# Optimization experiments

Hardware: AMD Instinct MI355X
Metric: run time of the kernel (lower is better)

Reference implementation:

```python
import jax, jax.numpy as jnp
import numpy as np

D_MODEL, D_FF, N_EXPERTS, TOP_K = 1024, 4096, 8, 2


def setup_inputs() -> dict:
    key = jax.random.key(0)
    k1, k2, k3, k4 = jax.random.split(key, 4)
    x = jax.random.normal(k1, (2, 2048, D_MODEL), dtype=jnp.float32)
    Wg = jax.random.normal(k2, (D_MODEL, N_EXPERTS), dtype=jnp.float32) * 0.02
    W1 = jax.random.normal(k3, (N_EXPERTS, D_MODEL, D_FF), dtype=jnp.float32) * 0.02
    b1 = jnp.zeros((N_EXPERTS, D_FF), dtype=jnp.float32)
    W2 = jax.random.normal(k4, (N_EXPERTS, D_FF, D_MODEL), dtype=jnp.float32) * 0.02
    b2 = jnp.zeros((N_EXPERTS, D_MODEL), dtype=jnp.float32)
    return {"x": x, "Wg": Wg, "W1": W1, "b1": b1, "W2": W2, "b2": b2}


def reference(x, Wg, W1, b1, W2, b2):
    B, S, D = x.shape
    T = B * S
    flat_x = x.reshape(T, D)                      # [T, D]
    # Router: softmax over expert logits, keep top-k experts per token.
    logits = flat_x @ Wg                          # [T, E]
    probs = jax.nn.softmax(logits, axis=-1)       # [T, E]
    _, top_idx = jax.lax.top_k(probs, TOP_K)      # [T, K]
    # mask[t, e] = 1 if expert e is among token t's top-k
    mask = jax.nn.one_hot(top_idx, N_EXPERTS, dtype=probs.dtype).sum(axis=1)  # [T, E]
    weights = probs * mask                        # gating score only for routed experts
    # Dense grouped expert MLP: every expert applied to all tokens, then masked-combined.
    h = jax.nn.gelu(jnp.einsum('td,edh->eth', flat_x, W1) + b1[:, None, :])  # [E, T, H]
    y = jnp.einsum('eth,ehd->etd', h, W2) + b2[:, None, :]                   # [E, T, D]
    out = jnp.einsum('etd,te->td', y, weights)                               # [T, D]
    return out.reshape(B, S, D)
```

## Files before the change

### kernel.cpp

```cpp
#include <hip/hip_runtime.h>
#include <hip/hip_bf16.h>

#define D_MODEL 1024
#define D_FF    4096
#define N_EXPERTS 8
#define TOPK    2
#define T_TOK   4096
#define NPAIR   (T_TOK * TOPK)
#define MT_MAX  32
#define KSPLIT  2

typedef __attribute__((ext_vector_type(8))) short s8v;
typedef __attribute__((ext_vector_type(4))) float f4v;
typedef __attribute__((ext_vector_type(4))) unsigned short u16x4;
typedef __attribute__((ext_vector_type(8))) unsigned short u16x8;

__device__ __forceinline__ void async16(const void* g, void* l) {
    __builtin_amdgcn_global_load_lds(
        (const __attribute__((address_space(1))) void*)g,
        (__attribute__((address_space(3))) void*)l, 16, 0, 0);
}

__device__ __forceinline__ float gelu_tanh(float v) {
    float u = 0.7978845608028654f * (v + 0.044715f * v * v * v);
    float t = 1.0f - 2.0f / (1.0f + __expf(2.0f * u));
    return 0.5f * v * (1.0f + t);
}

__device__ __forceinline__ unsigned short f2bf(float f) {
    union { __hip_bfloat16 b; unsigned short u; } cv;
    cv.b = __float2bfloat16(f);
    return cv.u;
}

__global__ __launch_bounds__(256) void router_kernel(
    const float* __restrict__ x, const float* __restrict__ Wg,
    int* __restrict__ top_e, float* __restrict__ top_w,
    __hip_bfloat16* __restrict__ xb)
{
    int wave = threadIdx.x >> 6;
    int lane = threadIdx.x & 63;
    int t = blockIdx.x * 4 + wave;
    if (t >= T_TOK) return;

    float acc[8] = {0.f,0.f,0.f,0.f,0.f,0.f,0.f,0.f};
    const float* xr = x + (size_t)t * D_MODEL;
    unsigned short* xbr = (unsigned short*)xb + (size_t)t * D_MODEL;
    #pragma unroll
    for (int it = 0; it < 4; it++) {
        int d0 = it * 256 + lane * 4;
        float4 xv = *(const float4*)(xr + d0);
        unsigned short bfv[4] = {f2bf(xv.x), f2bf(xv.y), f2bf(xv.z), f2bf(xv.w)};
        *(u16x4*)(xbr + d0) = *(u16x4*)bfv;
        float xa[4] = {xv.x, xv.y, xv.z, xv.w};
        #pragma unroll
        for (int u = 0; u < 4; u++) {
            const float* wr = Wg + (size_t)(d0 + u) * N_EXPERTS;
            float4 w0 = *(const float4*)wr;
            float4 w1 = *(const float4*)(wr + 4);
            acc[0] += xa[u] * w0.x; acc[1] += xa[u] * w0.y;
            acc[2] += xa[u] * w0.z; acc[3] += xa[u] * w0.w;
            acc[4] += xa[u] * w1.x; acc[5] += xa[u] * w1.y;
            acc[6] += xa[u] * w1.z; acc[7] += xa[u] * w1.w;
        }
    }
    #pragma unroll
    for (int off = 32; off >= 1; off >>= 1) {
        #pragma unroll
        for (int e = 0; e < 8; e++) acc[e] += __shfl_xor(acc[e], off);
    }
    if (lane == 0) {
        float m = acc[0];
        #pragma unroll
        for (int e = 1; e < 8; e++) m = fmaxf(m, acc[e]);
        float p[8]; float s = 0.f;
        #pragma unroll
        for (int e = 0; e < 8; e++) { p[e] = expf(acc[e] - m); s += p[e]; }
        float inv = 1.f / s;
        #pragma unroll
        for (int e = 0; e < 8; e++) p[e] *= inv;
        int i0 = 0; float b0 = p[0];
        #pragma unroll
        for (int e = 1; e < 8; e++) if (p[e] > b0) { b0 = p[e]; i0 = e; }
        int i1 = -1; float b1 = -1.f;
        #pragma unroll
        for (int e = 0; e < 8; e++) if (e != i0 && p[e] > b1) { b1 = p[e]; i1 = e; }
        top_e[2*t]   = i0; top_w[2*t]   = b0;
        top_e[2*t+1] = i1; top_w[2*t+1] = b1;
    }
}

__global__ __launch_bounds__(256) void setup_kernel(
    const int* __restrict__ top_e, int* __restrict__ offsets,
    int* __restrict__ pair_id)
{
    __shared__ int cnt[N_EXPERTS], base[N_EXPERTS], cur[N_EXPERTS];
    int tid = threadIdx.x;
    if (tid < N_EXPERTS) { cnt[tid] = 0; cur[tid] = 0; }
    __syncthreads();
    for (int i = tid; i < NPAIR; i += 256) atomicAdd(&cnt[top_e[i]], 1);
    __syncthreads();
    if (tid == 0) {
        int run = 0;
        #pragma unroll
        for (int e = 0; e < N_EXPERTS; e++) { base[e] = run; offsets[e] = run; run += cnt[e]; }
        offsets[N_EXPERTS] = run;
    }
    __syncthreads();
    for (int i = tid; i < NPAIR; i += 256) {
        int e = top_e[i];
        int pos = atomicAdd(&cur[e], 1);
        pair_id[base[e] + pos] = i;
    }
}

__global__ __launch_bounds__(256) void transpose_cast_kernel(
    const float* __restrict__ src, __hip_bfloat16* __restrict__ dst, int R, int C)
{
    int e = blockIdx.z;
    src += (size_t)e * R * C;
    dst += (size_t)e * R * C;
    int b0 = blockIdx.x * 64;
    int a0 = blockIdx.y * 64;

    __shared__ float tile[64][65];
    int tid = threadIdx.x;
    int lr = tid >> 4;
    int lc = (tid & 15) * 4;
    #pragma unroll
    for (int rr = 0; rr < 4; rr++) {
        int r = lr + rr * 16;
        *(float4*)&tile[r][lc] = *(const float4*)(src + (size_t)(a0 + r) * C + b0 + lc);
    }
    __syncthreads();
    int oc = tid >> 3;
    int oj = (tid & 7) * 8;
    #pragma unroll
    for (int rr = 0; rr < 2; rr++) {
        int c = oc + rr * 32;
        unsigned short t[8];
        #pragma unroll
        for (int j = 0; j < 8; j++) t[j] = f2bf(tile[oj + j][c]);
        *(u16x8*)((unsigned short*)dst + (size_t)(b0 + c) * R + a0 + oj) = *(u16x8*)t;
    }
}

__global__ __launch_bounds__(256) void gemm1_mfma(
    const __hip_bfloat16* __restrict__ xb, const __hip_bfloat16* __restrict__ W1T,
    const float* __restrict__ b1,
    const int* __restrict__ offsets, const int* __restrict__ pair_id,
    __hip_bfloat16* __restrict__ h)
{
    int e  = blockIdx.y >> 5;
    int mt = blockIdx.y & 31;
    int off_e = offsets[e];
    int cnt   = offsets[e + 1] - off_e;
    int m0 = mt * 128;
    if (m0 >= cnt) return;
    int n0 = blockIdx.x * 128;

    __shared__ __hip_bfloat16 As[128 * 32];
    __shared__ __hip_bfloat16 Bs[128 * 32];
    __shared__ int pid[128];

    int tid = threadIdx.x;
    if (tid < 128) {
        int r = m0 + tid; if (r >= cnt) r = cnt - 1;
        pid[tid] = pair_id[off_e + r];
    }
    __syncthreads();

    int lane = tid & 63, wid = tid >> 6;
    int c0 = tid, c1 = tid + 256;
    int r0 = ((c0 >> 6) << 4) | (c0 & 15), kb0 = (c0 >> 4) & 3;
    int r1 = ((c1 >> 6) << 4) | (c1 & 15), kb1 = (c1 >> 4) & 3;

    const __hip_bfloat16* gA0 = xb + (size_t)(pid[r0] >> 1) * D_MODEL + kb0 * 8;
    const __hip_bfloat16* gA1 = xb + (size_t)(pid[r1] >> 1) * D_MODEL + kb1 * 8;
    const __hip_bfloat16* WT  = W1T + (size_t)e * (D_MODEL * D_FF);
    const __hip_bfloat16* gB0 = WT + (size_t)(n0 + r0) * D_MODEL + kb0 * 8;
    const __hip_bfloat16* gB1 = WT + (size_t)(n0 + r1) * D_MODEL + kb1 * 8;

    int fm = lane & 15;
    int wm = (wid >> 1) * 64;
    int wn = (wid & 1) * 64;
    int rba = (wid >> 1) * 4;
    int rbb = (wid & 1) * 4;

    f4v acc[4][4];
    #pragma unroll
    for (int i = 0; i < 4; i++)
        #pragma unroll
        for (int j = 0; j < 4; j++)
            acc[i][j] = (f4v){0.f, 0.f, 0.f, 0.f};

    for (int k0 = 0; k0 < D_MODEL; k0 += 32) {
        async16(gA0 + k0, As + c0 * 8);
        async16(gA1 + k0, As + c1 * 8);
        async16(gB0 + k0, Bs + c0 * 8);
        async16(gB1 + k0, Bs + c1 * 8);
        __syncthreads();
        s8v af[4], bfr[4];
        #pragma unroll
        for (int i = 0; i < 4; i++)
            af[i] = *(const s8v*)(As + (rba + i) * 512 + lane * 8);
        #pragma unroll
        for (int j = 0; j < 4; j++)
            bfr[j] = *(const s8v*)(Bs + (rbb + j) * 512 + lane * 8);
        #pragma unroll
        for (int i = 0; i < 4; i++)
            #pragma unroll
            for (int j = 0; j < 4; j++)
                acc[i][j] = __builtin_amdgcn_mfma_f32_16x16x32_bf16(af[i], bfr[j], acc[i][j], 0, 0, 0);
        __syncthreads();
    }

    int rq = (lane >> 4) * 4;
    #pragma unroll
    for (int i = 0; i < 4; i++) {
        #pragma unroll
        for (int j = 0; j < 4; j++) {
            int n = n0 + wn + j * 16 + fm;
            float bias = b1[e * D_FF + n];
            #pragma unroll
            for (int r = 0; r < 4; r++) {
                int m = wm + i * 16 + rq + r;
                if (m0 + m < cnt) {
                    float v = acc[i][j][r] + bias;
                    h[(size_t)(off_e + m0 + m) * D_FF + n] = __float2bfloat16(gelu_tanh(v));
                }
            }
        }
    }
}

__global__ __launch_bounds__(256) void gemm2_mfma(
    const __hip_bfloat16* __restrict__ h, const __hip_bfloat16* __restrict__ W2T,
    const float* __restrict__ b2,
    const int* __restrict__ offsets, const int* __restrict__ pair_id,
    float* __restrict__ y0, float* __restrict__ y1)
{
    int e  = blockIdx.y >> 5;
    int mt = blockIdx.y & 31;
    int split = blockIdx.z;
    int off_e = offsets[e];
    int cnt   = offsets[e + 1] - off_e;
    int m0 = mt * 128;
    if (m0 >= cnt) return;
    int n0 = blockIdx.x * 128;

    __shared__ __hip_bfloat16 As[128 * 32];
    __shared__ __hip_bfloat16 Bs[128 * 32];
    __shared__ int pid[128];

    int tid = threadIdx.x;
    if (tid < 128) {
        int r = m0 + tid; if (r >= cnt) r = cnt - 1;
        pid[tid] = pair_id[off_e + r];
    }
    __syncthreads();

    int lane = tid & 63, wid = tid >> 6;
    int c0 = tid, c1 = tid + 256;
    int r0 = ((c0 >> 6) << 4) | (c0 & 15), kb0 = (c0 >> 4) & 3;
    int r1 = ((c1 >> 6) << 4) | (c1 & 15), kb1 = (c1 >> 4) & 3;
    int mr0 = m0 + r0; if (mr0 >= cnt) mr0 = cnt - 1;
    int mr1 = m0 + r1; if (mr1 >= cnt) mr1 = cnt - 1;

    const __hip_bfloat16* gA0 = h + (size_t)(off_e + mr0) * D_FF + kb0 * 8;
    const __hip_bfloat16* gA1 = h + (size_t)(off_e + mr1) * D_FF + kb1 * 8;
    const __hip_bfloat16* WT  = W2T + (size_t)e * (D_FF * D_MODEL);
    const __hip_bfloat16* gB0 = WT + (size_t)(n0 + r0) * D_FF + kb0 * 8;
    const __hip_bfloat16* gB1 = WT + (size_t)(n0 + r1) * D_FF + kb1 * 8;

    int fm = lane & 15;
    int wm = (wid >> 1) * 64;
    int wn = (wid & 1) * 64;
    int rba = (wid >> 1) * 4;
    int rbb = (wid & 1) * 4;

    f4v acc[4][4];
    #pragma unroll
    for (int i = 0; i < 4; i++)
        #pragma unroll
        for (int j = 0; j < 4; j++)
            acc[i][j] = (f4v){0.f, 0.f, 0.f, 0.f};

    const int KS = D_FF / KSPLIT;
    int kbase = split * KS;
    for (int k0 = kbase; k0 < kbase + KS; k0 += 32) {
        async16(gA0 + k0, As + c0 * 8);
        async16(gA1 + k0, As + c1 * 8);
        async16(gB0 + k0, Bs + c0 * 8);
        async16(gB1 + k0, Bs + c1 * 8);
        __syncthreads();
        s8v af[4], bfr[4];
        #pragma unroll
        for (int i = 0; i < 4; i++)
            af[i] = *(const s8v*)(As + (rba + i) * 512 + lane * 8);
        #pragma unroll
        for (int j = 0; j < 4; j++)
            bfr[j] = *(const s8v*)(Bs + (rbb + j) * 512 + lane * 8);
        #pragma unroll
        for (int i = 0; i < 4; i++)
            #pragma unroll
            for (int j = 0; j < 4; j++)
                acc[i][j] = __builtin_amdgcn_mfma_f32_16x16x32_bf16(af[i], bfr[j], acc[i][j], 0, 0, 0);
        __syncthreads();
    }

    float* yo = split ? y1 : y0;
    int rq = (lane >> 4) * 4;
    #pragma unroll
    for (int i = 0; i < 4; i++) {
        #pragma unroll
        for (int j = 0; j < 4; j++) {
            int n = n0 + wn + j * 16 + fm;
            float bias = split ? 0.f : b2[e * D_MODEL + n];
            #pragma unroll
            for (int r = 0; r < 4; r++) {
                int m = wm + i * 16 + rq + r;
                if (m0 + m < cnt) {
                    int p = pid[m];
                    yo[(size_t)p * D_MODEL + n] = acc[i][j][r] + bias;
                }
            }
        }
    }
}

__global__ __launch_bounds__(256) void combine_kernel(
    const float* __restrict__ y0, const float* __restrict__ y1,
    const float* __restrict__ top_w, float* __restrict__ out)
{
    int gid = blockIdx.x * blockDim.x + threadIdx.x;
    int t = gid >> 8;
    int c = gid & 255;
    float w0 = top_w[2*t];
    float w1 = top_w[2*t + 1];
    const float4* p0a = (const float4*)(y0 + (size_t)(2*t) * D_MODEL);
    const float4* p0b = (const float4*)(y1 + (size_t)(2*t) * D_MODEL);
    const float4* p1a = (const float4*)(y0 + (size_t)(2*t + 1) * D_MODEL);
    const float4* p1b = (const float4*)(y1 + (size_t)(2*t + 1) * D_MODEL);
    float4 a0 = p0a[c], a1 = p0b[c];
    float4 b0 = p1a[c], b1 = p1b[c];
    float4 o;
    o.x = w0*(a0.x + a1.x) + w1*(b0.x + b1.x);
    o.y = w0*(a0.y + a1.y) + w1*(b0.y + b1.y);
    o.z = w0*(a0.z + a1.z) + w1*(b0.z + b1.z);
    o.w = w0*(a0.w + a1.w) + w1*(b0.w + b1.w);
    ((float4*)out)[gid] = o;
}

extern "C" void kernel_launch(void* const* d_in, const int* in_sizes, int n_in,
                              void* d_out, int out_size, void* d_ws, size_t ws_size,
                              hipStream_t stream)
{
    const float* x  = (const float*)d_in[0];
    const float* Wg = (const float*)d_in[1];
    const float* W1 = (const float*)d_in[2];
    const float* b1 = (const float*)d_in[3];
    const float* W2 = (const float*)d_in[4];
    const float* b2 = (const float*)d_in[5];
    float* out = (float*)d_out;

    char* ws = (char*)d_ws;
    size_t off = 0;
    int*   top_e   = (int*)(ws + off);  off += (size_t)NPAIR * 4;
    float* top_w   = (float*)(ws + off); off += (size_t)NPAIR * 4;
    int*   offsets = (int*)(ws + off);  off += 256;
    int*   pair_id = (int*)(ws + off);  off += (size_t)NPAIR * 4;
    off = (off + 255) & ~(size_t)255;
    __hip_bfloat16* xb  = (__hip_bfloat16*)(ws + off); off += (size_t)T_TOK * D_MODEL * 2;
    __hip_bfloat16* W1T = (__hip_bfloat16*)(ws + off); off += (size_t)N_EXPERTS * D_MODEL * D_FF * 2;
    __hip_bfloat16* W2T = (__hip_bfloat16*)(ws + off); off += (size_t)N_EXPERTS * D_MODEL * D_FF * 2;
    __hip_bfloat16* h   = (__hip_bfloat16*)(ws + off); off += (size_t)NPAIR * D_FF * 2;
    float*          y   = (float*)(ws + off);          off += (size_t)NPAIR * D_MODEL * 4;

    float* ypart = (float*)W1T;

    router_kernel<<<T_TOK / 4, 256, 0, stream>>>(x, Wg, top_e, top_w, xb);
    setup_kernel<<<1, 256, 0, stream>>>(top_e, offsets, pair_id);

    transpose_cast_kernel<<<dim3(D_FF / 64, D_MODEL / 64, N_EXPERTS), 256, 0, stream>>>(
        W1, W1T, D_MODEL, D_FF);
    transpose_cast_kernel<<<dim3(D_MODEL / 64, D_FF / 64, N_EXPERTS), 256, 0, stream>>>(
        W2, W2T, D_FF, D_MODEL);

    gemm1_mfma<<<dim3(D_FF / 128, N_EXPERTS * MT_MAX), 256, 0, stream>>>(
        xb, W1T, b1, offsets, pair_id, h);
    gemm2_mfma<<<dim3(D_MODEL / 128, N_EXPERTS * MT_MAX, KSPLIT), 256, 0, stream>>>(
        h, W2T, b2, offsets, pair_id, y, ypart);
    combine_kernel<<<T_TOK, 256, 0, stream>>>(y, ypart, top_w, out);
}
```

Baseline: 717.0 us.

## Double-buffer LDS tiles in both expert GEMMs to overlap loads with MFMA

Both grouped GEMM kernels now use two LDS buffers per operand. The next K-tile is prefetched with async global-to-LDS loads while MFMAs run on the current tile, using a partial vmcnt wait and raw s_barrier in place of full __syncthreads. This targets the load latency that was exposed on every K step, at the cost of doubled LDS use per block, which may lower occupancy.

```diff
diff --git a/kernel.cpp b/kernel.cpp
--- a/kernel.cpp
+++ b/kernel.cpp
@@ -20,6 +20,9 @@
         (const __attribute__((address_space(1))) void*)g,
         (__attribute__((address_space(3))) void*)l, 16, 0, 0);
 }
+
+#define WAIT_VM(N) asm volatile("s_waitcnt vmcnt(" #N ")" ::: "memory")
+#define CFENCE()   asm volatile("" ::: "memory")
 
 __device__ __forceinline__ float gelu_tanh(float v) {
     float u = 0.7978845608028654f * (v + 0.044715f * v * v * v);
@@ -159,8 +162,8 @@
     if (m0 >= cnt) return;
     int n0 = blockIdx.x * 128;
 
-    __shared__ __hip_bfloat16 As[128 * 32];
-    __shared__ __hip_bfloat16 Bs[128 * 32];
+    __shared__ __hip_bfloat16 As[2][128 * 32];
+    __shared__ __hip_bfloat16 Bs[2][128 * 32];
     __shared__ int pid[128];
 
     int tid = threadIdx.x;
@@ -194,25 +197,55 @@
         for (int j = 0; j < 4; j++)
             acc[i][j] = (f4v){0.f, 0.f, 0.f, 0.f};
 
-    for (int k0 = 0; k0 < D_MODEL; k0 += 32) {
-        async16(gA0 + k0, As + c0 * 8);
-        async16(gA1 + k0, As + c1 * 8);
-        async16(gB0 + k0, Bs + c0 * 8);
-        async16(gB1 + k0, Bs + c1 * 8);
-        __syncthreads();
+    const int NT = D_MODEL / 32;
+
+    async16(gA0, As[0] + c0 * 8);
+    async16(gA1, As[0] + c1 * 8);
+    async16(gB0, Bs[0] + c0 * 8);
+    async16(gB1, Bs[0] + c1 * 8);
+
+    for (int t = 0; t + 1 < NT; ++t) {
+        int cur = t & 1, nxt = cur ^ 1;
+        int k1 = (t + 1) * 32;
+        async16(gA0 + k1, As[nxt] + c0 * 8);
+        async16(gA1 + k1, As[nxt] + c1 * 8);
+        async16(gB0 + k1, Bs[nxt] + c0 * 8);
+        async16(gB1 + k1, Bs[nxt] + c1 * 8);
+        WAIT_VM(4);
+        __builtin_amdgcn_s_barrier();
+        CFENCE();
         s8v af[4], bfr[4];
         #pragma unroll
         for (int i = 0; i < 4; i++)
-            af[i] = *(const s8v*)(As + (rba + i) * 512 + lane * 8);
-        #pragma unroll
-        for (int j = 0; j < 4; j++)
-            bfr[j] = *(const s8v*)(Bs + (rbb + j) * 512 + lane * 8);
+            af[i] = *(const s8v*)(As[cur] + (rba + i) * 512 + lane * 8);
+        #pragma unroll
+        for (int j = 0; j < 4; j++)
+            bfr[j] = *(const s8v*)(Bs[cur] + (rbb + j) * 512 + lane * 8);
         #pragma unroll
         for (int i = 0; i < 4; i++)
             #pragma unroll
             for (int j = 0; j < 4; j++)
                 acc[i][j] = __builtin_amdgcn_mfma_f32_16x16x32_bf16(af[i], bfr[j], acc[i][j], 0, 0, 0);
-        __syncthreads();
+        CFENCE();
+        __builtin_amdgcn_s_barrier();
+    }
+    {
+        int cur = (NT - 1) & 1;
+        WAIT_VM(0);
+        __builtin_amdgcn_s_barrier();
+        CFENCE();
+        s8v af[4], bfr[4];
+        #pragma unroll
+        for (int i = 0; i < 4; i++)
+            af[i] = *(const s8v*)(As[cur] + (rba + i) * 512 + lane * 8);
+        #pragma unroll
+        for (int j = 0; j < 4; j++)
+            bfr[j] = *(const s8v*)(Bs[cur] + (rbb + j) * 512 + lane * 8);
+        #pragma unroll
+        for (int i = 0; i < 4; i++)
+            #pragma unroll
+            for (int j = 0; j < 4; j++)
+                acc[i][j] = __builtin_amdgcn_mfma_f32_16x16x32_bf16(af[i], bfr[j], acc[i][j], 0, 0, 0);
     }
 
     int rq = (lane >> 4) * 4;
@@ -249,8 +282,8 @@
     if (m0 >= cnt) return;
     int n0 = blockIdx.x * 128;
 
-    __shared__ __hip_bfloat16 As[128 * 32];
-    __shared__ __hip_bfloat16 Bs[128 * 32];
+    __shared__ __hip_bfloat16 As[2][128 * 32];
+    __shared__ __hip_bfloat16 Bs[2][128 * 32];
     __shared__ int pid[128];
 
     int tid = threadIdx.x;
@@ -267,11 +300,14 @@
     int mr0 = m0 + r0; if (mr0 >= cnt) mr0 = cnt - 1;
     int mr1 = m0 + r1; if (mr1 >= cnt) mr1 = cnt - 1;
 
-    const __hip_bfloat16* gA0 = h + (size_t)(off_e + mr0) * D_FF + kb0 * 8;
-    const __hip_bfloat16* gA1 = h + (size_t)(off_e + mr1) * D_FF + kb1 * 8;
+    const int KS = D_FF / KSPLIT;
+    int kbase = split * KS;
+
+    const __hip_bfloat16* gA0 = h + (size_t)(off_e + mr0) * D_FF + kbase + kb0 * 8;
+    const __hip_bfloat16* gA1 = h + (size_t)(off_e + mr1) * D_FF + kbase + kb1 * 8;
     const __hip_bfloat16* WT  = W2T + (size_t)e * (D_FF * D_MODEL);
-    const __hip_bfloat16* gB0 = WT + (size_t)(n0 + r0) * D_FF + kb0 * 8;
-    const __hip_bfloat16* gB1 = WT + (size_t)(n0 + r1) * D_FF + kb1 * 8;
+    const __hip_bfloat16* gB0 = WT + (size_t)(n0 + r0) * D_FF + kbase + kb0 * 8;
+    const __hip_bfloat16* gB1 = WT + (size_t)(n0 + r1) * D_FF + kbase + kb1 * 8;
 
     int fm = lane & 15;
     int wm = (wid >> 1) * 64;
@@ -286,27 +322,55 @@
         for (int j = 0; j < 4; j++)
             acc[i][j] = (f4v){0.f, 0.f, 0.f, 0.f};
 
-    const int KS = D_FF / KSPLIT;
-    int kbase = split * KS;
-    for (int k0 = kbase; k0 < kbase + KS; k0 += 32) {
-        async16(gA0 + k0, As + c0 * 8);
-        async16(gA1 + k0, As + c1 * 8);
-        async16(gB0 + k0, Bs + c0 * 8);
-        async16(gB1 + k0, Bs + c1 * 8);
-        __syncthreads();
+    const int NT = KS / 32;
+
+    async16(gA0, As[0] + c0 * 8);
+    async16(gA1, As[0] + c1 * 8);
+    async16(gB0, Bs[0] + c0 * 8);
+    async16(gB1, Bs[0] + c1 * 8);
+
+    for (int t = 0; t + 1 < NT; ++t) {
+        int cur = t & 1, nxt = cur ^ 1;
+        int k1 = (t + 1) * 32;
+        async16(gA0 + k1, As[nxt] + c0 * 8);
+        async16(gA1 + k1, As[nxt] + c1 * 8);
+        async16(gB0 + k1, Bs[nxt] + c0 * 8);
+        async16(gB1 + k1, Bs[nxt] + c1 * 8);
+        WAIT_VM(4);
+        __builtin_amdgcn_s_barrier();
+        CFENCE();
         s8v af[4], bfr[4];
         #pragma unroll
         for (int i = 0; i < 4; i++)
-            af[i] = *(const s8v*)(As + (rba + i) * 512 + lane * 8);
-        #pragma unroll
-        for (int j = 0; j < 4; j++)
-            bfr[j] = *(const s8v*)(Bs + (rbb + j) * 512 + lane * 8);
+            af[i] = *(const s8v*)(As[cur] + (rba + i) * 512 + lane * 8);
+        #pragma unroll
+        for (int j = 0; j < 4; j++)
+            bfr[j] = *(const s8v*)(Bs[cur] + (rbb + j) * 512 + lane * 8);
         #pragma unroll
         for (int i = 0; i < 4; i++)
             #pragma unroll
             for (int j = 0; j < 4; j++)
                 acc[i][j] = __builtin_amdgcn_mfma_f32_16x16x32_bf16(af[i], bfr[j], acc[i][j], 0, 0, 0);
-        __syncthreads();
+        CFENCE();
+        __builtin_amdgcn_s_barrier();
+    }
+    {
+        int cur = (NT - 1) & 1;
+        WAIT_VM(0);
+        __builtin_amdgcn_s_barrier();
+        CFENCE();
+        s8v af[4], bfr[4];
+        #pragma unroll
+        for (int i = 0; i < 4; i++)
+            af[i] = *(const s8v*)(As[cur] + (rba + i) * 512 + lane * 8);
+        #pragma unroll
+        for (int j = 0; j < 4; j++)
+            bfr[j] = *(const s8v*)(Bs[cur] + (rbb + j) * 512 + lane * 8);
+        #pragma unroll
+        for (int i = 0; i < 4; i++)
+            #pragma unroll
+            for (int j = 0; j < 4; j++)
+                acc[i][j] = __builtin_amdgcn_mfma_f32_16x16x32_bf16(af[i], bfr[j], acc[i][j], 0, 0, 0);
     }
 
     float* yo = split ? y1 : y0;
```

Result: no change. 718.9 us (+0.3%).
